# Optimization experiments

Measured on AMD Instinct MI355X. Metric: run time of the kernel, lower is better.

The kernel has to match this reference:

```python
import jax, jax.numpy as jnp
import numpy as np

B, CN, DEG, IN_F, OUT_F, K = 32, 1024, 2, 128, 128, 10
NODES = [1, 16, 128, 1024]


def setup_inputs() -> dict:
    key = jax.random.key(0)
    ks = jax.random.split(key, 16)
    d = {}
    for i, n in enumerate(NODES):
        d[f"tree{i}"] = jax.random.normal(ks[i], (B, n, IN_F), dtype=jnp.float32)
    for i in range(4):
        d[f"Uw{i}"] = jax.random.normal(ks[4 + i], (IN_F, OUT_F), dtype=jnp.float32) * 0.05
        d[f"Ub{i}"] = jnp.zeros((OUT_F,), dtype=jnp.float32)
    d["W_up"] = jax.random.normal(ks[8], (CN, IN_F, DEG * IN_F), dtype=jnp.float32) * 0.05
    d["Fw0"] = jax.random.normal(ks[9], (IN_F, K * IN_F), dtype=jnp.float32) * 0.05
    d["Fb0"] = jnp.zeros((K * IN_F,), dtype=jnp.float32)
    d["Fw1"] = jax.random.normal(ks[10], (K * IN_F, OUT_F), dtype=jnp.float32) * 0.05
    d["Fb1"] = jnp.zeros((OUT_F,), dtype=jnp.float32)
    d["b_bias"] = jax.random.normal(ks[11], (1, DEG * CN, OUT_F), dtype=jnp.float32) * 0.05
    return d


def reference(tree0, tree1, tree2, tree3,
              Uw0, Ub0, Uw1, Ub1, Uw2, Ub2, Uw3, Ub3,
              W_up, Fw0, Fb0, Fw1, Fb1, b_bias):
    tree = [tree0, tree1, tree2, tree3]
    Uw = [Uw0, Uw1, Uw2, Uw3]
    Ub = [Ub0, Ub1, Ub2, Ub3]
    curr_node = W_up.shape[0]
    in_feat = W_up.shape[1]
    degree = W_up.shape[2] // in_feat

    # Ancestor info: project each depth, then tile each ancestor node's
    # projected vector to cover its descendants at the current level.
    anc = jnp.zeros((tree[0].shape[0], curr_node, Uw0.shape[1]), dtype=tree0.dtype)
    for t, w, b in zip(tree, Uw, Ub):
        Q = t @ w + b                       # [B, anc_node, out_feat]
        rep = curr_node // t.shape[1]
        anc = anc + jnp.repeat(Q, rep, axis=1)  # == tf.tile([1,1,rep]) + reshape

    # Per-node unique-weight upsample: [B,n,1,in] @ [n,in,deg*in]
    nl = jnp.einsum('bni,nio->bno', tree[-1], W_up)            # [B, CN, deg*in]
    nl = nl.reshape(nl.shape[0], curr_node * degree, in_feat)   # [B, CN*deg, in]
    nl = (nl @ Fw0 + Fb0) @ Fw1 + Fb1                           # Dense chain
    nl = nl + jnp.repeat(anc, degree, axis=1)                   # broadcast ancestors
    nl = nl + b_bias
    return jnp.where(nl >= 0, nl, 0.2 * nl)                     # LeakyReLU(0.2)
```

## Files before the change

kernel.cpp:

```cpp
#include <hip/hip_runtime.h>
#include <stdint.h>


using short8   = __attribute__((ext_vector_type(8))) short;
using floatx16 = __attribute__((ext_vector_type(16))) float;

__device__ __forceinline__ unsigned short f2bf(float f) {
    unsigned int u = __builtin_bit_cast(unsigned int, f);
    return (unsigned short)((u + 0x8000u) >> 16);
}

__device__ __forceinline__ short8 cvt8(const float* p) {
    const float4 v0 = *reinterpret_cast<const float4*>(p);
    const float4 v1 = *reinterpret_cast<const float4*>(p + 4);
    short8 a;
    a[0] = (short)f2bf(v0.x); a[1] = (short)f2bf(v0.y);
    a[2] = (short)f2bf(v0.z); a[3] = (short)f2bf(v0.w);
    a[4] = (short)f2bf(v1.x); a[5] = (short)f2bf(v1.y);
    a[6] = (short)f2bf(v1.z); a[7] = (short)f2bf(v1.w);
    return a;
}

#define QS_OFF  0
#define FB_OFF  524288
#define FF_OFF  524416
#define UW_OFF  532608

__global__ __launch_bounds__(256) void ffused_p1(
    const float* __restrict__ Fw0, const float* __restrict__ Fb0,
    const float* __restrict__ Fw1, float* __restrict__ P)
{
    const int kc = blockIdx.x;
    const int i  = blockIdx.y;
    const int j  = threadIdx.x & 127;
    const int il = threadIdx.x >> 7;
    const int k0 = kc * 160 + il * 80;
    const float* __restrict__ src = (i < 128) ? (Fw0 + (size_t)i * 1280) : Fb0;
    float acc = 0.f;
    #pragma unroll 8
    for (int kk = 0; kk < 80; ++kk)
        acc += src[k0 + kk] * Fw1[(size_t)(k0 + kk) * 128 + j];
    P[(size_t)(kc * 2 + il) * 16512 + i * 128 + j] = acc;
}

__global__ __launch_bounds__(256) void ffused_p2(
    const float* __restrict__ P, const float* __restrict__ Fb1,
    unsigned short* __restrict__ FfusedBF, float* __restrict__ Fbias)
{
    const int idx = blockIdx.x * 256 + threadIdx.x;
    if (idx >= 16512) return;
    const int i = idx >> 7, j = idx & 127;
    float s = 0.f;
    #pragma unroll
    for (int p = 0; p < 16; ++p) s += P[(size_t)p * 16512 + idx];
    if (i < 128) FfusedBF[(((i >> 3) * 128) + j) * 8 + (i & 7)] = f2bf(s);
    else         Fbias[j] = s + Fb1[j];
}

__global__ __launch_bounds__(256) void uwbf_kernel(
    const float* __restrict__ Uw0, const float* __restrict__ Uw1,
    const float* __restrict__ Uw2, const float* __restrict__ Uw3,
    unsigned short* __restrict__ UwBF)
{
    const int mat = blockIdx.x >> 4;
    const int kg  = blockIdx.x & 15;
    const float* __restrict__ Uw = (mat == 0) ? Uw0 : (mat == 1) ? Uw1
                                 : (mat == 2) ? Uw2 : Uw3;
    const int col = threadIdx.x & 127;
    const int kh  = threadIdx.x >> 7;
    #pragma unroll
    for (int q = 0; q < 4; ++q) {
        const int kk = kh * 4 + q;
        const float v = Uw[(size_t)(kg * 8 + kk) * 128 + col];
        UwBF[(((size_t)(mat * 16 + kg) * 128) + col) * 8 + kk] = f2bf(v);
    }
}

__global__ __launch_bounds__(256) void qsum_kernel(
    const float* __restrict__ t0, const float* __restrict__ t1,
    const float* __restrict__ t2, const unsigned short* __restrict__ UwBF,
    float* __restrict__ Qsum)
{
    const int i2   = blockIdx.x;
    const int tid  = threadIdx.x;
    const int w    = tid >> 6;
    const int lane = tid & 63;
    const int l31  = lane & 31;
    const int half = lane >> 5;
    const int colq = w * 32 + l31;
    const int b    = l31;

    floatx16 acc;
    #pragma unroll
    for (int r = 0; r < 16; ++r) acc[r] = 0.f;

    #pragma unroll
    for (int mi = 0; mi < 3; ++mi) {
        const float* base; int row;
        if      (mi == 0) { base = t0; row = b; }
        else if (mi == 1) { base = t1; row = b * 16 + (i2 >> 3); }
        else              { base = t2; row = b * 128 + i2; }
        const float* rp = base + (size_t)row * 128;
        #pragma unroll
        for (int k8 = 0; k8 < 8; ++k8) {
            const short8 a  = cvt8(rp + k8 * 16 + half * 8);
            const short8 bf = *reinterpret_cast<const short8*>(
                &UwBF[(((size_t)(mi * 16 + 2 * k8 + half) * 128) + colq) * 8]);
            acc = __builtin_amdgcn_mfma_f32_32x32x16_bf16(a, bf, acc, 0, 0, 0);
        }
    }
    #pragma unroll
    for (int r = 0; r < 16; ++r) {
        const int brow = (r & 3) + 8 * (r >> 2) + 4 * half;
        Qsum[((size_t)brow * 128 + i2) * 128 + colq] = acc[r];
    }
}

__global__ __launch_bounds__(256, 2) void tree_main(
    const float* __restrict__ t3,
    const float* __restrict__ Ub0, const float* __restrict__ Ub1,
    const float* __restrict__ Ub2, const float* __restrict__ Ub3,
    const float* __restrict__ Wup, const float* __restrict__ bbias,
    const unsigned short* __restrict__ FfusedBF,
    const unsigned short* __restrict__ UwBF,
    const float* __restrict__ Fbias, const float* __restrict__ Qsum,
    float* __restrict__ out)
{
    const int n    = blockIdx.x;
    const int tid  = threadIdx.x;
    const int w    = tid >> 6;
    const int lane = tid & 63;
    const int l31  = lane & 31;
    const int half = lane >> 5;
    const int colq = w * 32 + l31;

    __shared__ __align__(16) unsigned char smem_raw[16640];
    unsigned short* T3lds = (unsigned short*)smem_raw;
    unsigned short* Ulds  = (unsigned short*)smem_raw;

    #pragma unroll
    for (int i = 0; i < 4; ++i) {
        const int idx = i * 256 + tid;
        const int b   = idx >> 5;
        const int q   = idx & 31;
        const float4 v = *reinterpret_cast<const float4*>(
            t3 + ((size_t)b * 1024 + n) * 128 + q * 4);
        ushort4 u;
        u.x = f2bf(v.x); u.y = f2bf(v.y); u.z = f2bf(v.z); u.w = f2bf(v.w);
        *reinterpret_cast<ushort4*>(&T3lds[((q >> 1) * 33 + b) * 8 + (q & 1) * 4]) = u;
    }
    __syncthreads();

    floatx16 qacc, accT0, accT1;
    #pragma unroll
    for (int r = 0; r < 16; ++r) { qacc[r] = 0.f; accT0[r] = 0.f; accT1[r] = 0.f; }

    const float* __restrict__ Wp0 = Wup + (size_t)n * 32768 + (half * 8) * 256 + w * 64 + l31;
    const float* __restrict__ Wp1 = Wp0 + 32;

    float p0[8], p1[8];
    #pragma unroll
    for (int jj = 0; jj < 8; ++jj) { p0[jj] = Wp0[jj * 256]; p1[jj] = Wp1[jj * 256]; }

    #pragma unroll
    for (int ks = 0; ks < 8; ++ks) {
        float n0[8], n1[8];
        if (ks < 7) {
            const int koff = (ks + 1) * 16 * 256;
            #pragma unroll
            for (int jj = 0; jj < 8; ++jj) {
                n0[jj] = Wp0[koff + jj * 256];
                n1[jj] = Wp1[koff + jj * 256];
            }
        }
        const short8 afk = *reinterpret_cast<const short8*>(
            &T3lds[((2 * ks + half) * 33 + l31) * 8]);
        const short8 bfu = *reinterpret_cast<const short8*>(
            &UwBF[(((size_t)(48 + 2 * ks + half) * 128) + colq) * 8]);
        short8 a0, a1;
        #pragma unroll
        for (int jj = 0; jj < 8; ++jj) {
            a0[jj] = (short)f2bf(p0[jj]);
            a1[jj] = (short)f2bf(p1[jj]);
        }
        qacc  = __builtin_amdgcn_mfma_f32_32x32x16_bf16(afk, bfu, qacc, 0, 0, 0);
        accT0 = __builtin_amdgcn_mfma_f32_32x32x16_bf16(a0, afk, accT0, 0, 0, 0);
        accT1 = __builtin_amdgcn_mfma_f32_32x32x16_bf16(a1, afk, accT1, 0, 0, 0);
        #pragma unroll
        for (int jj = 0; jj < 8; ++jj) { p0[jj] = n0[jj]; p1[jj] = n1[jj]; }
    }
    __syncthreads();

    #pragma unroll
    for (int tt = 0; tt < 2; ++tt) {
        const floatx16 Av = tt ? accT1 : accT0;
        #pragma unroll
        for (int r = 0; r < 16; ++r) {
            const int cm = w * 64 + tt * 32 + ((r & 3) + 8 * (r >> 2) + 4 * half);
            const int d  = cm >> 7;
            const int cp = cm & 127;
            Ulds[(((cp >> 3) * 65) + d * 32 + l31) * 8 + (cp & 7)] = f2bf(Av[r]);
        }
    }
    __syncthreads();

    floatx16 o0, o1;
    #pragma unroll
    for (int r = 0; r < 16; ++r) { o0[r] = 0.f; o1[r] = 0.f; }
    #pragma unroll
    for (int ks = 0; ks < 8; ++ks) {
        const int kg2 = 2 * ks + half;
        const short8 a0 = *reinterpret_cast<const short8*>(&Ulds[(kg2 * 65 + l31) * 8]);
        const short8 a1 = *reinterpret_cast<const short8*>(&Ulds[(kg2 * 65 + 32 + l31) * 8]);
        const short8 bf = *reinterpret_cast<const short8*>(
            &FfusedBF[(((size_t)kg2 * 128) + colq) * 8]);
        o0 = __builtin_amdgcn_mfma_f32_32x32x16_bf16(a0, bf, o0, 0, 0, 0);
        o1 = __builtin_amdgcn_mfma_f32_32x32x16_bf16(a1, bf, o1, 0, 0, 0);
    }

    const float ubsum = Ub0[colq] + Ub1[colq] + Ub2[colq] + Ub3[colq] + Fbias[colq];
    const float bb0 = bbias[(size_t)(2 * n + 0) * 128 + colq];
    const float bb1 = bbias[(size_t)(2 * n + 1) * 128 + colq];
    const int i2 = n >> 3;
    #pragma unroll
    for (int r = 0; r < 16; ++r) {
        const int brow = (r & 3) + 8 * (r >> 2) + 4 * half;
        const float addc = qacc[r] + ubsum + Qsum[((size_t)brow * 128 + i2) * 128 + colq];
        float v0 = o0[r] + addc + bb0;
        float v1 = o1[r] + addc + bb1;
        v0 = (v0 >= 0.f) ? v0 : 0.2f * v0;
        v1 = (v1 >= 0.f) ? v1 : 0.2f * v1;
        const size_t idx0 = ((size_t)brow * 2048 + 2 * n) * 128 + colq;
        out[idx0]       = v0;
        out[idx0 + 128] = v1;
    }
}

extern "C" void kernel_launch(void* const* d_in, const int* in_sizes, int n_in,
                              void* d_out, int out_size, void* d_ws, size_t ws_size,
                              hipStream_t stream) {
    const float* t0  = (const float*)d_in[0];
    const float* t1  = (const float*)d_in[1];
    const float* t2  = (const float*)d_in[2];
    const float* t3  = (const float*)d_in[3];
    const float* Uw0 = (const float*)d_in[4];
    const float* Ub0 = (const float*)d_in[5];
    const float* Uw1 = (const float*)d_in[6];
    const float* Ub1 = (const float*)d_in[7];
    const float* Uw2 = (const float*)d_in[8];
    const float* Ub2 = (const float*)d_in[9];
    const float* Uw3 = (const float*)d_in[10];
    const float* Ub3 = (const float*)d_in[11];
    const float* Wup = (const float*)d_in[12];
    const float* Fw0 = (const float*)d_in[13];
    const float* Fb0 = (const float*)d_in[14];
    const float* Fw1 = (const float*)d_in[15];
    const float* Fb1 = (const float*)d_in[16];
    const float* bb  = (const float*)d_in[17];

    float* ws = (float*)d_ws;
    float* Qsum           = ws + QS_OFF;
    float* Fbias          = ws + FB_OFF;
    unsigned short* FfBF  = (unsigned short*)(ws + FF_OFF);
    unsigned short* UwBF  = (unsigned short*)(ws + UW_OFF);

    ffused_p1<<<dim3(8, 129), 256, 0, stream>>>(Fw0, Fb0, Fw1, Qsum);
    ffused_p2<<<65, 256, 0, stream>>>(Qsum, Fb1, FfBF, Fbias);
    uwbf_kernel<<<64, 256, 0, stream>>>(Uw0, Uw1, Uw2, Uw3, UwBF);
    qsum_kernel<<<128, 256, 0, stream>>>(t0, t1, t2, UwBF, Qsum);
    tree_main<<<1024, 256, 0, stream>>>(t3,
                                        Ub0, Ub1, Ub2, Ub3,
                                        Wup, bb, FfBF, UwBF, Fbias, Qsum,
                                        (float*)d_out);
}
```

Measured before the change: 283.8 us.

## Stage qsum A tiles in LDS, transpose Qsum layout, prefetch Qsum early

qsum_kernel now has all 256 threads cooperatively load the t0/t1/t2 rows with float4 reads, convert them to bf16 once, and store them in padded LDS. Previously each of the four waves loaded and converted the same rows redundantly. Qsum is stored in an i2-major layout, so tree_main reads contiguous 32x128 blocks, and those loads plus the bias loads are issued before the final MFMA loop to hide their latency. In exchange qsum_kernel uses extra LDS and a barrier, and tree_main holds 16 more live registers.

```diff
diff --git a/kernel.cpp b/kernel.cpp
--- a/kernel.cpp
+++ b/kernel.cpp
@@ -8,17 +8,6 @@
 __device__ __forceinline__ unsigned short f2bf(float f) {
     unsigned int u = __builtin_bit_cast(unsigned int, f);
     return (unsigned short)((u + 0x8000u) >> 16);
-}
-
-__device__ __forceinline__ short8 cvt8(const float* p) {
-    const float4 v0 = *reinterpret_cast<const float4*>(p);
-    const float4 v1 = *reinterpret_cast<const float4*>(p + 4);
-    short8 a;
-    a[0] = (short)f2bf(v0.x); a[1] = (short)f2bf(v0.y);
-    a[2] = (short)f2bf(v0.z); a[3] = (short)f2bf(v0.w);
-    a[4] = (short)f2bf(v1.x); a[5] = (short)f2bf(v1.y);
-    a[6] = (short)f2bf(v1.z); a[7] = (short)f2bf(v1.w);
-    return a;
 }
 
 #define QS_OFF  0
@@ -88,31 +77,46 @@
     const int l31  = lane & 31;
     const int half = lane >> 5;
     const int colq = w * 32 + l31;
-    const int b    = l31;
+
+    __shared__ __align__(16) unsigned short Alds[48 * 33 * 8];
+
+    #pragma unroll
+    for (int mi = 0; mi < 3; ++mi) {
+        const float* __restrict__ base = (mi == 0) ? t0 : (mi == 1) ? t1 : t2;
+        #pragma unroll
+        for (int i = 0; i < 4; ++i) {
+            const int idx = i * 256 + tid;
+            const int b   = idx >> 5;
+            const int q   = idx & 31;
+            int row;
+            if      (mi == 0) row = b;
+            else if (mi == 1) row = b * 16 + (i2 >> 3);
+            else              row = b * 128 + i2;
+            const float4 v = *reinterpret_cast<const float4*>(
+                base + (size_t)row * 128 + q * 4);
+            ushort4 u;
+            u.x = f2bf(v.x); u.y = f2bf(v.y); u.z = f2bf(v.z); u.w = f2bf(v.w);
+            const int kg = mi * 16 + (q >> 1);
+            *reinterpret_cast<ushort4*>(&Alds[(kg * 33 + b) * 8 + (q & 1) * 4]) = u;
+        }
+    }
+    __syncthreads();
 
     floatx16 acc;
     #pragma unroll
     for (int r = 0; r < 16; ++r) acc[r] = 0.f;
-
-    #pragma unroll
-    for (int mi = 0; mi < 3; ++mi) {
-        const float* base; int row;
-        if      (mi == 0) { base = t0; row = b; }
-        else if (mi == 1) { base = t1; row = b * 16 + (i2 >> 3); }
-        else              { base = t2; row = b * 128 + i2; }
-        const float* rp = base + (size_t)row * 128;
-        #pragma unroll
-        for (int k8 = 0; k8 < 8; ++k8) {
-            const short8 a  = cvt8(rp + k8 * 16 + half * 8);
-            const short8 bf = *reinterpret_cast<const short8*>(
-                &UwBF[(((size_t)(mi * 16 + 2 * k8 + half) * 128) + colq) * 8]);
-            acc = __builtin_amdgcn_mfma_f32_32x32x16_bf16(a, bf, acc, 0, 0, 0);
-        }
+    #pragma unroll
+    for (int ks = 0; ks < 24; ++ks) {
+        const int kg = 2 * ks + half;
+        const short8 a = *reinterpret_cast<const short8*>(&Alds[(kg * 33 + l31) * 8]);
+        const short8 bf = *reinterpret_cast<const short8*>(
+            &UwBF[(((size_t)kg * 128) + colq) * 8]);
+        acc = __builtin_amdgcn_mfma_f32_32x32x16_bf16(a, bf, acc, 0, 0, 0);
     }
     #pragma unroll
     for (int r = 0; r < 16; ++r) {
         const int brow = (r & 3) + 8 * (r >> 2) + 4 * half;
-        Qsum[((size_t)brow * 128 + i2) * 128 + colq] = acc[r];
+        Qsum[((size_t)i2 * 32 + brow) * 128 + colq] = acc[r];
     }
 }
 
@@ -204,6 +208,17 @@
     }
     __syncthreads();
 
+    const int i2 = n >> 3;
+    float qs[16];
+    #pragma unroll
+    for (int r = 0; r < 16; ++r) {
+        const int brow = (r & 3) + 8 * (r >> 2) + 4 * half;
+        qs[r] = Qsum[((size_t)i2 * 32 + brow) * 128 + colq];
+    }
+    const float ubsum = Ub0[colq] + Ub1[colq] + Ub2[colq] + Ub3[colq] + Fbias[colq];
+    const float bb0 = bbias[(size_t)(2 * n + 0) * 128 + colq];
+    const float bb1 = bbias[(size_t)(2 * n + 1) * 128 + colq];
+
     floatx16 o0, o1;
     #pragma unroll
     for (int r = 0; r < 16; ++r) { o0[r] = 0.f; o1[r] = 0.f; }
@@ -218,14 +233,10 @@
         o1 = __builtin_amdgcn_mfma_f32_32x32x16_bf16(a1, bf, o1, 0, 0, 0);
     }
 
-    const float ubsum = Ub0[colq] + Ub1[colq] + Ub2[colq] + Ub3[colq] + Fbias[colq];
-    const float bb0 = bbias[(size_t)(2 * n + 0) * 128 + colq];
-    const float bb1 = bbias[(size_t)(2 * n + 1) * 128 + colq];
-    const int i2 = n >> 3;
     #pragma unroll
     for (int r = 0; r < 16; ++r) {
         const int brow = (r & 3) + 8 * (r >> 2) + 4 * half;
-        const float addc = qacc[r] + ubsum + Qsum[((size_t)brow * 128 + i2) * 128 + colq];
+        const float addc = qacc[r] + ubsum + qs[r];
         float v0 = o0[r] + addc + bb0;
         float v1 = o1[r] + addc + bb1;
         v0 = (v0 >= 0.f) ? v0 : 0.2f * v0;
```

New measurement: 268.1 us. 1.06x faster.
